# Performance work log

Measured on AMD Instinct MI355X. Metric: run time of the kernel, lower is better.

## Reference

```python
import jax, jax.numpy as jnp
import numpy as np

B, S, D, H = 16, 1024, 256, 8
DEPTH = D // H          # 32
H2 = H // 2             # 4 heads per branch
DH = D // 2             # 128 per-branch model dim


def setup_inputs() -> dict:
    key = jax.random.key(0)
    ks = jax.random.split(key, 20)
    f32 = jnp.float32
    q_ori = jax.random.normal(ks[0], (B, S, D), f32)
    k_ori = jax.random.normal(ks[1], (B, S, D), f32)
    v_ori = jax.random.normal(ks[2], (B, S, D), f32)
    mask = (jax.random.uniform(ks[3], (B, 1, 1, S)) < 0.1).astype(f32)
    # adjacency: sparse 0/1 graph structure
    adj = (jax.random.uniform(ks[4], (B, S, S)) < 0.05).astype(f32)
    # distance matrix: positive values, softmaxed inside the dist branch
    dist = jax.random.uniform(ks[5], (B, S, S), dtype=f32)

    def dense(k, din, dout):
        return jax.random.normal(k, (din, dout), f32) * 0.02

    params = {
        'Wq_dist': dense(ks[6], D, DH), 'bq_dist': jnp.zeros((DH,), f32),
        'Wk_dist': dense(ks[7], D, DH), 'bk_dist': jnp.zeros((DH,), f32),
        'Wv_dist': dense(ks[8], D, DH), 'bv_dist': jnp.zeros((DH,), f32),
        'Wq_adj': dense(ks[9], D, DH), 'bq_adj': jnp.zeros((DH,), f32),
        'Wk_adj': dense(ks[10], D, DH), 'bk_adj': jnp.zeros((DH,), f32),
        'Wv_adj': dense(ks[11], D, DH), 'bv_adj': jnp.zeros((DH,), f32),
        'Wo': dense(ks[12], D, D), 'bo': jnp.zeros((D,), f32),
    }
    return dict(v_ori=v_ori, k_ori=k_ori, q_ori=q_ori, mask=mask,
                adj=adj, dist=dist, **params)


def _split_heads(x):
    # (B, S, DH) -> (B, H2, S, DEPTH)
    b, s, _ = x.shape
    return x.reshape(b, s, H2, DEPTH).transpose(0, 2, 1, 3)


def _sdpa_AD(q, k, v, mask, adj=None, dist=None):
    neg = mask * (-1e9)                                   # (B,1,1,S)
    scale = 1.0 / jnp.sqrt(jnp.asarray(DEPTH, q.dtype))
    logits = jnp.einsum('bhqd,bhkd->bhqk', q, k) * scale + neg
    w = jax.nn.softmax(logits, axis=-1)                   # (B,H2,S,S)
    if adj is not None:
        w = w * adj[:, None]                              # multiplicative adjacency reweight
    if dist is not None:
        w = w * jax.nn.softmax(dist[:, None] + neg, axis=-1)
    out = jnp.einsum('bhqk,bhkd->bhqd', w, v)
    return out, w


def reference(v_ori, k_ori, q_ori, mask, adj, dist,
              Wq_dist, bq_dist, Wk_dist, bk_dist, Wv_dist, bv_dist,
              Wq_adj, bq_adj, Wk_adj, bk_adj, Wv_adj, bv_adj, Wo, bo):
    b = q_ori.shape[0]
    # dist branch
    q = _split_heads(q_ori @ Wq_dist + bq_dist)
    k = _split_heads(k_ori @ Wk_dist + bk_dist)
    v = _split_heads(v_ori @ Wv_dist + bv_dist)
    o_dist, w_dist = _sdpa_AD(q, k, v, mask, adj=None, dist=dist)
    o_dist = o_dist.transpose(0, 2, 1, 3).reshape(b, -1, DH)
    # adj branch
    q = _split_heads(q_ori @ Wq_adj + bq_adj)
    k = _split_heads(k_ori @ Wk_adj + bk_adj)
    v = _split_heads(v_ori @ Wv_adj + bv_adj)
    o_adj, w_adj = _sdpa_AD(q, k, v, mask, adj=adj, dist=None)
    o_adj = o_adj.transpose(0, 2, 1, 3).reshape(b, -1, DH)

    concat = jnp.concatenate([o_dist, o_adj], axis=-1)    # (B,S,D)
    attn_w = jnp.concatenate([w_dist, w_adj], axis=1)     # (B,H,S,S)
    output = concat @ Wo + bo                             # (B,S,D)
    return output, attn_w
```

## Files before the change

### kernel.cpp

```cpp
#include <hip/hip_runtime.h>
#include <cstddef>

static constexpr int BB = 16, SS = 1024, DD = 256;
static constexpr size_t OUTW = (size_t)BB * SS * DD;
#define SCALE 0.17677669529663687f

__global__ __launch_bounds__(256) void pack_kernel(
    const float* __restrict__ Wqd, const float* __restrict__ Wqa,
    const float* __restrict__ Wkd, const float* __restrict__ Wka,
    const float* __restrict__ Wvd, const float* __restrict__ Wva,
    const float* __restrict__ bqd, const float* __restrict__ bqa,
    const float* __restrict__ bkd, const float* __restrict__ bka,
    const float* __restrict__ bvd, const float* __restrict__ bva,
    float* __restrict__ Wcat, float* __restrict__ bcat)
{
  int i = blockIdx.x * 256 + threadIdx.x;
  if (i < 3 * 256 * 256) {
    int g = i >> 16, r = (i >> 8) & 255, n = i & 255;
    const float* W0 = (g == 0) ? Wqd : (g == 1) ? Wkd : Wvd;
    const float* W1 = (g == 0) ? Wqa : (g == 1) ? Wka : Wva;
    Wcat[i] = (n < 128) ? W0[r * 128 + n] : W1[r * 128 + (n - 128)];
  } else {
    int j = i - 3 * 256 * 256;
    if (j < 3 * 256) {
      int g = j >> 8, n = j & 255;
      const float* b0 = (g == 0) ? bqd : (g == 1) ? bkd : bvd;
      const float* b1 = (g == 0) ? bqa : (g == 1) ? bka : bva;
      bcat[j] = (n < 128) ? b0[n] : b1[n - 128];
    }
  }
}

__device__ __forceinline__ void gemm_body(
    const float* __restrict__ X, const float* __restrict__ W,
    const float* __restrict__ bias, float* __restrict__ Y)
{
  __shared__ float As[2][16][132];
  __shared__ float Bs[2][16][132];
  const int t = threadIdx.x;
  const int m0 = blockIdx.x * 128;
  const int n0 = blockIdx.y * 128;
  const int tm = t >> 4, tn = t & 15;
  const int rA = t >> 1;
  const int hA = (t & 1) * 8;
  const int kB = t >> 4;
  const int qB = t & 15;

  float acc[8][8];
#pragma unroll
  for (int i = 0; i < 8; ++i)
#pragma unroll
    for (int j = 0; j < 8; ++j) acc[i][j] = 0.f;

  const float* xrow = X + (size_t)(m0 + rA) * 256;

  {
    float4 a0 = *(const float4*)&xrow[hA];
    float4 a1 = *(const float4*)&xrow[hA + 4];
    float4 b0 = *(const float4*)&W[(size_t)kB * 256 + n0 + 4 * qB];
    float4 b1 = *(const float4*)&W[(size_t)kB * 256 + n0 + 64 + 4 * qB];
    As[0][hA + 0][rA] = a0.x; As[0][hA + 1][rA] = a0.y;
    As[0][hA + 2][rA] = a0.z; As[0][hA + 3][rA] = a0.w;
    As[0][hA + 4][rA] = a1.x; As[0][hA + 5][rA] = a1.y;
    As[0][hA + 6][rA] = a1.z; As[0][hA + 7][rA] = a1.w;
    *(float4*)&Bs[0][kB][4 * qB] = b0;
    *(float4*)&Bs[0][kB][64 + 4 * qB] = b1;
  }
  __syncthreads();

  int cur = 0;
  for (int k0 = 0; k0 < 256; k0 += 16) {
    const bool more = (k0 + 16) < 256;
    float4 na0 = {0,0,0,0}, na1 = {0,0,0,0}, nb0 = {0,0,0,0}, nb1 = {0,0,0,0};
    if (more) {
      na0 = *(const float4*)&xrow[k0 + 16 + hA];
      na1 = *(const float4*)&xrow[k0 + 16 + hA + 4];
      nb0 = *(const float4*)&W[(size_t)(k0 + 16 + kB) * 256 + n0 + 4 * qB];
      nb1 = *(const float4*)&W[(size_t)(k0 + 16 + kB) * 256 + n0 + 64 + 4 * qB];
    }
#pragma unroll
    for (int kk = 0; kk < 16; ++kk) {
      float4 av0 = *(const float4*)&As[cur][kk][8 * tm];
      float4 av1 = *(const float4*)&As[cur][kk][8 * tm + 4];
      float4 bv0 = *(const float4*)&Bs[cur][kk][8 * tn];
      float4 bv1 = *(const float4*)&Bs[cur][kk][8 * tn + 4];
      float ar[8] = {av0.x, av0.y, av0.z, av0.w, av1.x, av1.y, av1.z, av1.w};
      float br[8] = {bv0.x, bv0.y, bv0.z, bv0.w, bv1.x, bv1.y, bv1.z, bv1.w};
#pragma unroll
      for (int i = 0; i < 8; ++i)
#pragma unroll
        for (int j = 0; j < 8; ++j) acc[i][j] = fmaf(ar[i], br[j], acc[i][j]);
    }
    if (more) {
      const int nxt = cur ^ 1;
      As[nxt][hA + 0][rA] = na0.x; As[nxt][hA + 1][rA] = na0.y;
      As[nxt][hA + 2][rA] = na0.z; As[nxt][hA + 3][rA] = na0.w;
      As[nxt][hA + 4][rA] = na1.x; As[nxt][hA + 5][rA] = na1.y;
      As[nxt][hA + 6][rA] = na1.z; As[nxt][hA + 7][rA] = na1.w;
      *(float4*)&Bs[nxt][kB][4 * qB] = nb0;
      *(float4*)&Bs[nxt][kB][64 + 4 * qB] = nb1;
      __syncthreads();
      cur = nxt;
    }
  }

  float4 bb0 = *(const float4*)&bias[n0 + 8 * tn];
  float4 bb1 = *(const float4*)&bias[n0 + 8 * tn + 4];
#pragma unroll
  for (int i = 0; i < 8; ++i) {
    float4 o0, o1;
    o0.x = acc[i][0] + bb0.x; o0.y = acc[i][1] + bb0.y;
    o0.z = acc[i][2] + bb0.z; o0.w = acc[i][3] + bb0.w;
    o1.x = acc[i][4] + bb1.x; o1.y = acc[i][5] + bb1.y;
    o1.z = acc[i][6] + bb1.z; o1.w = acc[i][7] + bb1.w;
    float* yr = &Y[(size_t)(m0 + 8 * tm + i) * 256 + n0 + 8 * tn];
    *(float4*)&yr[0] = o0;
    *(float4*)&yr[4] = o1;
  }
}

__global__ __launch_bounds__(256, 3) void gemm_qkv_kernel(
    const float* __restrict__ q, const float* __restrict__ k,
    const float* __restrict__ v, const float* __restrict__ Wcat,
    const float* __restrict__ bcat, float* __restrict__ Yb)
{
  const int z = blockIdx.z;
  const float* X = (z == 0) ? q : (z == 1) ? k : v;
  gemm_body(X, Wcat + z * 65536, bcat + (z << 8), Yb + (size_t)z * 4194304);
}

__global__ __launch_bounds__(256, 3) void gemm_out_kernel(
    const float* __restrict__ X, const float* __restrict__ W,
    const float* __restrict__ bias, float* __restrict__ Y)
{
  gemm_body(X, W, bias, Y);
}

__global__ __launch_bounds__(256) void dist_stats_kernel(
    const float* __restrict__ dist, const float* __restrict__ mask,
    float* __restrict__ dinv)
{
  const int t = threadIdx.x;
  const int w = t >> 6, lane = t & 63;
  const int row = blockIdx.x * 4 + w;
  const int b = row >> 10;
  const float* dr = dist + (size_t)row * 1024;
  const float* mr = mask + b * 1024;
  float s = 0.f;
#pragma unroll
  for (int j = 0; j < 16; ++j) {
    int c = lane + 64 * j;
    s += __expf(dr[c] - 1e9f * mr[c]);
  }
#pragma unroll
  for (int off = 32; off >= 1; off >>= 1) s += __shfl_xor(s, off);
  if (lane == 0) dinv[row] = 1.0f / s;
}

__global__ __launch_bounds__(256, 2) void attn_fused_kernel(
    const float* __restrict__ Qc, const float* __restrict__ Kc,
    const float* __restrict__ Vc, const float* __restrict__ mask,
    const float* __restrict__ adj, const float* __restrict__ dist,
    const float* __restrict__ dinv,
    float* __restrict__ wout, float* __restrict__ conc)
{
  __shared__ float Ls[16384];
  __shared__ float KVs[64][36];
  const int t = threadIdx.x;
  const int bid = blockIdx.x;
  const int qb = bid & 63, h = (bid >> 6) & 7, b = bid >> 9;
  const int q0 = qb * 16;
  const int branch = h >> 2;
  const int boff = branch * 128 + (h & 3) * 32;
  const int wv = t >> 6, l = t & 63;
  const int gr = q0 + 4 * wv;
  const int sr = t >> 2, sq = t & 3;

  float Q[4][32];
  const float* qbase = Qc + ((size_t)(b * 1024 + gr)) * 256 + boff;
#pragma unroll
  for (int r = 0; r < 4; ++r)
#pragma unroll
    for (int dq = 0; dq < 8; ++dq) {
      float4 a = *(const float4*)&qbase[(size_t)r * 256 + 4 * dq];
      Q[r][4 * dq + 0] = a.x; Q[r][4 * dq + 1] = a.y;
      Q[r][4 * dq + 2] = a.z; Q[r][4 * dq + 3] = a.w;
    }

  const float* kb = Kc + (size_t)(b * 1024) * 256 + boff;
  const float* mr = mask + b * 1024;

  float sp0 = 0.f, sp1 = 0.f, sp2 = 0.f, sp3 = 0.f;
  {
    float4 ka  = *(const float4*)&kb[(size_t)sr * 256 + 4 * sq];
    float4 kc2 = *(const float4*)&kb[(size_t)sr * 256 + 16 + 4 * sq];
    *(float4*)&KVs[sr][4 * sq] = ka;
    *(float4*)&KVs[sr][16 + 4 * sq] = kc2;
    __syncthreads();
  }
  float ngc = -1e9f * mr[l];
  for (int cc = 0; cc < 16; ++cc) {
    float4 nka, nkc2; float nng = 0.f;
    if (cc < 15) {
      const int cn0 = (cc + 1) * 64;
      nka  = *(const float4*)&kb[(size_t)(cn0 + sr) * 256 + 4 * sq];
      nkc2 = *(const float4*)&kb[(size_t)(cn0 + sr) * 256 + 16 + 4 * sq];
      nng = -1e9f * mr[cn0 + l];
    }
    const int c = cc * 64 + l;
    float s0 = 0.f, s1 = 0.f, s2 = 0.f, s3 = 0.f;
#pragma unroll
    for (int dq = 0; dq < 8; ++dq) {
      float4 kv = *(const float4*)&KVs[l][4 * dq];
      s0 = fmaf(Q[0][4 * dq + 0], kv.x, s0); s0 = fmaf(Q[0][4 * dq + 1], kv.y, s0);
      s0 = fmaf(Q[0][4 * dq + 2], kv.z, s0); s0 = fmaf(Q[0][4 * dq + 3], kv.w, s0);
      s1 = fmaf(Q[1][4 * dq + 0], kv.x, s1); s1 = fmaf(Q[1][4 * dq + 1], kv.y, s1);
      s1 = fmaf(Q[1][4 * dq + 2], kv.z, s1); s1 = fmaf(Q[1][4 * dq + 3], kv.w, s1);
      s2 = fmaf(Q[2][4 * dq + 0], kv.x, s2); s2 = fmaf(Q[2][4 * dq + 1], kv.y, s2);
      s2 = fmaf(Q[2][4 * dq + 2], kv.z, s2); s2 = fmaf(Q[2][4 * dq + 3], kv.w, s2);
      s3 = fmaf(Q[3][4 * dq + 0], kv.x, s3); s3 = fmaf(Q[3][4 * dq + 1], kv.y, s3);
      s3 = fmaf(Q[3][4 * dq + 2], kv.z, s3); s3 = fmaf(Q[3][4 * dq + 3], kv.w, s3);
    }
    float e0 = __expf(fmaf(s0, SCALE, ngc));
    float e1 = __expf(fmaf(s1, SCALE, ngc));
    float e2 = __expf(fmaf(s2, SCALE, ngc));
    float e3 = __expf(fmaf(s3, SCALE, ngc));
    Ls[(4 * wv + 0) * 1024 + c] = e0;
    Ls[(4 * wv + 1) * 1024 + c] = e1;
    Ls[(4 * wv + 2) * 1024 + c] = e2;
    Ls[(4 * wv + 3) * 1024 + c] = e3;
    sp0 += e0; sp1 += e1; sp2 += e2; sp3 += e3;
    if (cc < 15) {
      __syncthreads();
      *(float4*)&KVs[sr][4 * sq] = nka;
      *(float4*)&KVs[sr][16 + 4 * sq] = nkc2;
      __syncthreads();
      ngc = nng;
    }
  }

#pragma unroll
  for (int off = 32; off >= 1; off >>= 1) {
    sp0 += __shfl_xor(sp0, off);
    sp1 += __shfl_xor(sp1, off);
    sp2 += __shfl_xor(sp2, off);
    sp3 += __shfl_xor(sp3, off);
  }
  float inv[4] = {1.0f / sp0, 1.0f / sp1, 1.0f / sp2, 1.0f / sp3};

  float o[4][32];
#pragma unroll
  for (int r = 0; r < 4; ++r)
#pragma unroll
    for (int d = 0; d < 32; ++d) o[r][d] = 0.f;

  const float* br_[4];
  float din[4];
  if (branch == 0) {
#pragma unroll
    for (int r = 0; r < 4; ++r) {
      din[r] = dinv[b * 1024 + gr + r];
      br_[r] = dist + (size_t)(b * 1024 + gr + r) * 1024;
    }
  } else {
#pragma unroll
    for (int r = 0; r < 4; ++r) {
      din[r] = 0.f;
      br_[r] = adj + (size_t)(b * 1024 + gr + r) * 1024;
    }
  }
  const float* vb = Vc + (size_t)(b * 1024) * 256 + boff;
  const size_t wr0 = ((size_t)(b * 8 + h) * 1024 + gr) * 1024;

  float fpre[4], ngc2;
  {
    float4 va  = *(const float4*)&vb[(size_t)sr * 256 + 4 * sq];
    float4 vc2 = *(const float4*)&vb[(size_t)sr * 256 + 16 + 4 * sq];
#pragma unroll
    for (int r = 0; r < 4; ++r) fpre[r] = br_[r][l];
    ngc2 = -1e9f * mr[l];
    __syncthreads();
    *(float4*)&KVs[sr][4 * sq] = va;
    *(float4*)&KVs[sr][16 + 4 * sq] = vc2;
    __syncthreads();
  }
  for (int cc = 0; cc < 16; ++cc) {
    const int c = cc * 64 + l;
    float4 nva, nvc2; float nf[4]; float nng = 0.f;
    if (cc < 15) {
      const int cn0 = (cc + 1) * 64;
      nva  = *(const float4*)&vb[(size_t)(cn0 + sr) * 256 + 4 * sq];
      nvc2 = *(const float4*)&vb[(size_t)(cn0 + sr) * 256 + 16 + 4 * sq];
#pragma unroll
      for (int r = 0; r < 4; ++r) nf[r] = br_[r][cn0 + l];
      nng = -1e9f * mr[cn0 + l];
    }
    float w[4];
#pragma unroll
    for (int r = 0; r < 4; ++r) {
      float e = Ls[(4 * wv + r) * 1024 + c] * inv[r];
      float f;
      if (branch == 0) f = __expf(fpre[r] + ngc2) * din[r];
      else             f = fpre[r];
      w[r] = e * f;
      __builtin_nontemporal_store(w[r], &wout[wr0 + (size_t)r * 1024 + c]);
    }
#pragma unroll
    for (int dq = 0; dq < 8; ++dq) {
      float4 vv = *(const float4*)&KVs[l][4 * dq];
      o[0][4 * dq + 0] = fmaf(w[0], vv.x, o[0][4 * dq + 0]);
      o[0][4 * dq + 1] = fmaf(w[0], vv.y, o[0][4 * dq + 1]);
      o[0][4 * dq + 2] = fmaf(w[0], vv.z, o[0][4 * dq + 2]);
      o[0][4 * dq + 3] = fmaf(w[0], vv.w, o[0][4 * dq + 3]);
      o[1][4 * dq + 0] = fmaf(w[1], vv.x, o[1][4 * dq + 0]);
      o[1][4 * dq + 1] = fmaf(w[1], vv.y, o[1][4 * dq + 1]);
      o[1][4 * dq + 2] = fmaf(w[1], vv.z, o[1][4 * dq + 2]);
      o[1][4 * dq + 3] = fmaf(w[1], vv.w, o[1][4 * dq + 3]);
      o[2][4 * dq + 0] = fmaf(w[2], vv.x, o[2][4 * dq + 0]);
      o[2][4 * dq + 1] = fmaf(w[2], vv.y, o[2][4 * dq + 1]);
      o[2][4 * dq + 2] = fmaf(w[2], vv.z, o[2][4 * dq + 2]);
      o[2][4 * dq + 3] = fmaf(w[2], vv.w, o[2][4 * dq + 3]);
      o[3][4 * dq + 0] = fmaf(w[3], vv.x, o[3][4 * dq + 0]);
      o[3][4 * dq + 1] = fmaf(w[3], vv.y, o[3][4 * dq + 1]);
      o[3][4 * dq + 2] = fmaf(w[3], vv.z, o[3][4 * dq + 2]);
      o[3][4 * dq + 3] = fmaf(w[3], vv.w, o[3][4 * dq + 3]);
    }
    if (cc < 15) {
      __syncthreads();
      *(float4*)&KVs[sr][4 * sq] = nva;
      *(float4*)&KVs[sr][16 + 4 * sq] = nvc2;
      __syncthreads();
#pragma unroll
      for (int r = 0; r < 4; ++r) fpre[r] = nf[r];
      ngc2 = nng;
    }
  }

  {
    float* Ws_ = &Ls[wv * 4096];
#pragma unroll
    for (int p = 0; p < 2; ++p) {
#pragma unroll
      for (int j = 0; j < 32; ++j) {
        const int r = j >> 4, d2 = j & 15;
        const int slot = (j + l) & 31;
        float2 u;
        u.x = o[2 * p + r][2 * d2];
        u.y = o[2 * p + r][2 * d2 + 1];
        *(float2*)&Ws_[l * 64 + 2 * slot] = u;
      }
      const int rp = l >> 5, d = l & 31;
      const int jc = rp * 16 + (d >> 1);
      float a = 0.f;
#pragma unroll
      for (int ll = 0; ll < 64; ++ll)
        a += Ws_[ll * 64 + 2 * ((jc + ll) & 31) + (d & 1)];
      conc[((size_t)(b * 1024) + q0 + 4 * wv + 2 * p + rp) * 256 + boff + d] = a;
    }
  }
}

extern "C" void kernel_launch(void* const* d_in, const int* in_sizes, int n_in,
                              void* d_out, int out_size, void* d_ws, size_t ws_size,
                              hipStream_t stream)
{
  const float* v_ori = (const float*)d_in[0];
  const float* k_ori = (const float*)d_in[1];
  const float* q_ori = (const float*)d_in[2];
  const float* mask  = (const float*)d_in[3];
  const float* adj   = (const float*)d_in[4];
  const float* dist  = (const float*)d_in[5];
  const float* Wqd = (const float*)d_in[6];  const float* bqd = (const float*)d_in[7];
  const float* Wkd = (const float*)d_in[8];  const float* bkd = (const float*)d_in[9];
  const float* Wvd = (const float*)d_in[10]; const float* bvd = (const float*)d_in[11];
  const float* Wqa = (const float*)d_in[12]; const float* bqa = (const float*)d_in[13];
  const float* Wka = (const float*)d_in[14]; const float* bka = (const float*)d_in[15];
  const float* Wva = (const float*)d_in[16]; const float* bva = (const float*)d_in[17];
  const float* Wo  = (const float*)d_in[18]; const float* bo  = (const float*)d_in[19];

  float* out = (float*)d_out;
  float* ws  = (float*)d_ws;
  float* Qc    = ws;
  float* Kc    = Qc + 4194304;
  float* Vc    = Kc + 4194304;
  float* conc  = Vc + 4194304;
  float* dinvb = conc + 4194304;
  float* Wcat  = dinvb + 16384;
  float* bcat  = Wcat + 196608;

  pack_kernel<<<771, 256, 0, stream>>>(Wqd, Wqa, Wkd, Wka, Wvd, Wva,
                                       bqd, bqa, bkd, bka, bvd, bva, Wcat, bcat);
  gemm_qkv_kernel<<<dim3(128, 2, 3), 256, 0, stream>>>(q_ori, k_ori, v_ori,
                                                       Wcat, bcat, Qc);
  dist_stats_kernel<<<4096, 256, 0, stream>>>(dist, mask, dinvb);
  attn_fused_kernel<<<8192, 256, 0, stream>>>(Qc, Kc, Vc, mask, adj, dist,
                                              dinvb, out + OUTW, conc);
  gemm_out_kernel<<<dim3(128, 2), 256, 0, stream>>>(conc, Wo, bo, out);
}
```

Measured before the change: 1.370 ms.

## Restructure projection GEMMs to keep full-K weight slice in LDS

Replaces the 128x128 double-buffered tiled GEMM with a 128x32 output tile. Each block preloads the entire 256x32 weight slice into shared memory once, then streams X rows straight from global memory with register prefetch. This removes the per-k-step LDS staging and barriers of X and quadruples the grid to 1024/3072 blocks for better occupancy. The cost is that X is re-read from global/L2 eight times, once per column block, and each thread does less register-level reuse with only a 4x4 accumulator.

```diff
diff --git a/kernel.cpp b/kernel.cpp
--- a/kernel.cpp
+++ b/kernel.cpp
@@ -35,91 +35,100 @@
     const float* __restrict__ X, const float* __restrict__ W,
     const float* __restrict__ bias, float* __restrict__ Y)
 {
-  __shared__ float As[2][16][132];
-  __shared__ float Bs[2][16][132];
+  __shared__ float Wl[256 * 32];
   const int t = threadIdx.x;
   const int m0 = blockIdx.x * 128;
-  const int n0 = blockIdx.y * 128;
-  const int tm = t >> 4, tn = t & 15;
-  const int rA = t >> 1;
-  const int hA = (t & 1) * 8;
-  const int kB = t >> 4;
-  const int qB = t & 15;
-
-  float acc[8][8];
-#pragma unroll
-  for (int i = 0; i < 8; ++i)
-#pragma unroll
-    for (int j = 0; j < 8; ++j) acc[i][j] = 0.f;
-
-  const float* xrow = X + (size_t)(m0 + rA) * 256;
-
+  const int n0 = blockIdx.y * 32;
+  const int tr = t >> 3;
+  const int tc4 = (t & 7) * 4;
+
+#pragma unroll
+  for (int i = 0; i < 8; ++i) {
+    const int k = (t >> 3) + 32 * i;
+    *(float4*)&Wl[k * 32 + tc4] = *(const float4*)&W[(size_t)k * 256 + n0 + tc4];
+  }
+  __syncthreads();
+
+  float acc[4][4];
+#pragma unroll
+  for (int i = 0; i < 4; ++i)
+#pragma unroll
+    for (int j = 0; j < 4; ++j) acc[i][j] = 0.f;
+
+  const float* xr = X + (size_t)(m0 + 4 * tr) * 256;
+
+  float4 a[4], an[4];
+#pragma unroll
+  for (int r = 0; r < 4; ++r) a[r] = *(const float4*)&xr[r * 256];
+
+#pragma unroll 2
+  for (int k = 0; k < 252; k += 4) {
+#pragma unroll
+    for (int r = 0; r < 4; ++r) an[r] = *(const float4*)&xr[r * 256 + k + 4];
+    float4 w0 = *(const float4*)&Wl[(k + 0) * 32 + tc4];
+    float4 w1 = *(const float4*)&Wl[(k + 1) * 32 + tc4];
+    float4 w2 = *(const float4*)&Wl[(k + 2) * 32 + tc4];
+    float4 w3 = *(const float4*)&Wl[(k + 3) * 32 + tc4];
+#pragma unroll
+    for (int r = 0; r < 4; ++r) {
+      acc[r][0] = fmaf(a[r].x, w0.x, acc[r][0]);
+      acc[r][1] = fmaf(a[r].x, w0.y, acc[r][1]);
+      acc[r][2] = fmaf(a[r].x, w0.z, acc[r][2]);
+      acc[r][3] = fmaf(a[r].x, w0.w, acc[r][3]);
+      acc[r][0] = fmaf(a[r].y, w1.x, acc[r][0]);
+      acc[r][1] = fmaf(a[r].y, w1.y, acc[r][1]);
+      acc[r][2] = fmaf(a[r].y, w1.z, acc[r][2]);
+      acc[r][3] = fmaf(a[r].y, w1.w, acc[r][3]);
+      acc[r][0] = fmaf(a[r].z, w2.x, acc[r][0]);
+      acc[r][1] = fmaf(a[r].z, w2.y, acc[r][1]);
+      acc[r][2] = fmaf(a[r].z, w2.z, acc[r][2]);
+      acc[r][3] = fmaf(a[r].z, w2.w, acc[r][3]);
+      acc[r][0] = fmaf(a[r].w, w3.x, acc[r][0]);
+      acc[r][1] = fmaf(a[r].w, w3.y, acc[r][1]);
+      acc[r][2] = fmaf(a[r].w, w3.z, acc[r][2]);
+      acc[r][3] = fmaf(a[r].w, w3.w, acc[r][3]);
+    }
+#pragma unroll
+    for (int r = 0; r < 4; ++r) a[r] = an[r];
+  }
   {
-    float4 a0 = *(const float4*)&xrow[hA];
-    float4 a1 = *(const float4*)&xrow[hA + 4];
-    float4 b0 = *(const float4*)&W[(size_t)kB * 256 + n0 + 4 * qB];
-    float4 b1 = *(const float4*)&W[(size_t)kB * 256 + n0 + 64 + 4 * qB];
-    As[0][hA + 0][rA] = a0.x; As[0][hA + 1][rA] = a0.y;
-    As[0][hA + 2][rA] = a0.z; As[0][hA + 3][rA] = a0.w;
-    As[0][hA + 4][rA] = a1.x; As[0][hA + 5][rA] = a1.y;
-    As[0][hA + 6][rA] = a1.z; As[0][hA + 7][rA] = a1.w;
-    *(float4*)&Bs[0][kB][4 * qB] = b0;
-    *(float4*)&Bs[0][kB][64 + 4 * qB] = b1;
-  }
-  __syncthreads();
-
-  int cur = 0;
-  for (int k0 = 0; k0 < 256; k0 += 16) {
-    const bool more = (k0 + 16) < 256;
-    float4 na0 = {0,0,0,0}, na1 = {0,0,0,0}, nb0 = {0,0,0,0}, nb1 = {0,0,0,0};
-    if (more) {
-      na0 = *(const float4*)&xrow[k0 + 16 + hA];
-      na1 = *(const float4*)&xrow[k0 + 16 + hA + 4];
-      nb0 = *(const float4*)&W[(size_t)(k0 + 16 + kB) * 256 + n0 + 4 * qB];
-      nb1 = *(const float4*)&W[(size_t)(k0 + 16 + kB) * 256 + n0 + 64 + 4 * qB];
-    }
-#pragma unroll
-    for (int kk = 0; kk < 16; ++kk) {
-      float4 av0 = *(const float4*)&As[cur][kk][8 * tm];
-      float4 av1 = *(const float4*)&As[cur][kk][8 * tm + 4];
-      float4 bv0 = *(const float4*)&Bs[cur][kk][8 * tn];
-      float4 bv1 = *(const float4*)&Bs[cur][kk][8 * tn + 4];
-      float ar[8] = {av0.x, av0.y, av0.z, av0.w, av1.x, av1.y, av1.z, av1.w};
-      float br[8] = {bv0.x, bv0.y, bv0.z, bv0.w, bv1.x, bv1.y, bv1.z, bv1.w};
-#pragma unroll
-      for (int i = 0; i < 8; ++i)
-#pragma unroll
-        for (int j = 0; j < 8; ++j) acc[i][j] = fmaf(ar[i], br[j], acc[i][j]);
-    }
-    if (more) {
-      const int nxt = cur ^ 1;
-      As[nxt][hA + 0][rA] = na0.x; As[nxt][hA + 1][rA] = na0.y;
-      As[nxt][hA + 2][rA] = na0.z; As[nxt][hA + 3][rA] = na0.w;
-      As[nxt][hA + 4][rA] = na1.x; As[nxt][hA + 5][rA] = na1.y;
-      As[nxt][hA + 6][rA] = na1.z; As[nxt][hA + 7][rA] = na1.w;
-      *(float4*)&Bs[nxt][kB][4 * qB] = nb0;
-      *(float4*)&Bs[nxt][kB][64 + 4 * qB] = nb1;
-      __syncthreads();
-      cur = nxt;
-    }
-  }
-
-  float4 bb0 = *(const float4*)&bias[n0 + 8 * tn];
-  float4 bb1 = *(const float4*)&bias[n0 + 8 * tn + 4];
-#pragma unroll
-  for (int i = 0; i < 8; ++i) {
-    float4 o0, o1;
-    o0.x = acc[i][0] + bb0.x; o0.y = acc[i][1] + bb0.y;
-    o0.z = acc[i][2] + bb0.z; o0.w = acc[i][3] + bb0.w;
-    o1.x = acc[i][4] + bb1.x; o1.y = acc[i][5] + bb1.y;
-    o1.z = acc[i][6] + bb1.z; o1.w = acc[i][7] + bb1.w;
-    float* yr = &Y[(size_t)(m0 + 8 * tm + i) * 256 + n0 + 8 * tn];
-    *(float4*)&yr[0] = o0;
-    *(float4*)&yr[4] = o1;
-  }
-}
-
-__global__ __launch_bounds__(256, 3) void gemm_qkv_kernel(
+    const int k = 252;
+    float4 w0 = *(const float4*)&Wl[(k + 0) * 32 + tc4];
+    float4 w1 = *(const float4*)&Wl[(k + 1) * 32 + tc4];
+    float4 w2 = *(const float4*)&Wl[(k + 2) * 32 + tc4];
+    float4 w3 = *(const float4*)&Wl[(k + 3) * 32 + tc4];
+#pragma unroll
+    for (int r = 0; r < 4; ++r) {
+      acc[r][0] = fmaf(a[r].x, w0.x, acc[r][0]);
+      acc[r][1] = fmaf(a[r].x, w0.y, acc[r][1]);
+      acc[r][2] = fmaf(a[r].x, w0.z, acc[r][2]);
+      acc[r][3] = fmaf(a[r].x, w0.w, acc[r][3]);
+      acc[r][0] = fmaf(a[r].y, w1.x, acc[r][0]);
+      acc[r][1] = fmaf(a[r].y, w1.y, acc[r][1]);
+      acc[r][2] = fmaf(a[r].y, w1.z, acc[r][2]);
+      acc[r][3] = fmaf(a[r].y, w1.w, acc[r][3]);
+      acc[r][0] = fmaf(a[r].z, w2.x, acc[r][0]);
+      acc[r][1] = fmaf(a[r].z, w2.y, acc[r][1]);
+      acc[r][2] = fmaf(a[r].z, w2.z, acc[r][2]);
+      acc[r][3] = fmaf(a[r].z, w2.w, acc[r][3]);
+      acc[r][0] = fmaf(a[r].w, w3.x, acc[r][0]);
+      acc[r][1] = fmaf(a[r].w, w3.y, acc[r][1]);
+      acc[r][2] = fmaf(a[r].w, w3.z, acc[r][2]);
+      acc[r][3] = fmaf(a[r].w, w3.w, acc[r][3]);
+    }
+  }
+
+  const float4 bb = *(const float4*)&bias[n0 + tc4];
+#pragma unroll
+  for (int r = 0; r < 4; ++r) {
+    float4 o;
+    o.x = acc[r][0] + bb.x; o.y = acc[r][1] + bb.y;
+    o.z = acc[r][2] + bb.z; o.w = acc[r][3] + bb.w;
+    *(float4*)&Y[(size_t)(m0 + 4 * tr + r) * 256 + n0 + tc4] = o;
+  }
+}
+
+__global__ __launch_bounds__(256, 4) void gemm_qkv_kernel(
     const float* __restrict__ q, const float* __restrict__ k,
     const float* __restrict__ v, const float* __restrict__ Wcat,
     const float* __restrict__ bcat, float* __restrict__ Yb)
@@ -129,7 +138,7 @@
   gemm_body(X, Wcat + z * 65536, bcat + (z << 8), Yb + (size_t)z * 4194304);
 }
 
-__global__ __launch_bounds__(256, 3) void gemm_out_kernel(
+__global__ __launch_bounds__(256, 4) void gemm_out_kernel(
     const float* __restrict__ X, const float* __restrict__ W,
     const float* __restrict__ bias, float* __restrict__ Y)
 {
@@ -390,10 +399,10 @@
 
   pack_kernel<<<771, 256, 0, stream>>>(Wqd, Wqa, Wkd, Wka, Wvd, Wva,
                                        bqd, bqa, bkd, bka, bvd, bva, Wcat, bcat);
-  gemm_qkv_kernel<<<dim3(128, 2, 3), 256, 0, stream>>>(q_ori, k_ori, v_ori,
+  gemm_qkv_kernel<<<dim3(128, 8, 3), 256, 0, stream>>>(q_ori, k_ori, v_ori,
                                                        Wcat, bcat, Qc);
   dist_stats_kernel<<<4096, 256, 0, stream>>>(dist, mask, dinvb);
   attn_fused_kernel<<<8192, 256, 0, stream>>>(Qc, Kc, Vc, mask, adj, dist,
                                               dinvb, out + OUTW, conc);
-  gemm_out_kernel<<<dim3(128, 2), 256, 0, stream>>>(conc, Wo, bo, out);
-}
+  gemm_out_kernel<<<dim3(128, 8), 256, 0, stream>>>(conc, Wo, bo, out);
+}
```

Result: faster. 1.190 ms (-13.1%).
